# Kernel optimization log

Hardware: AMD Instinct MI355X
Metric: run time of the kernel (lower is better)

## Reference

```python
import jax, jax.numpy as jnp
import numpy as np
from jax.scipy.special import erf, erfc

B, D, C = 256, 512, 85742

def setup_inputs() -> dict:
    key = jax.random.key(0)
    k1, k2, k3, k4, k5 = jax.random.split(key, 5)
    x = jax.random.normal(k1, (B, D), dtype=jnp.float32)
    mu = jax.random.normal(k2, (B, D), dtype=jnp.float32)
    std = jax.random.uniform(k3, (B, D), dtype=jnp.float32)
    weight = jax.random.normal(k4, (C, D), dtype=jnp.float32)
    label = jax.random.randint(k5, (B,), 0, C, dtype=jnp.int64)
    return {"x": x, "mu": mu, "std": std, "weight": weight, "label": label}


def reference(x, mu, std, weight, label):
    # one_hot: [B, C] float, as in F.one_hot(...).float()
    one_hot = jax.nn.one_hot(label, weight.shape[0], dtype=jnp.float32)
    # wy = one_hot @ weight (embedding gather expressed as GEMM), wi = (1 - one_hot) @ weight
    wy = one_hot @ weight                 # [B, D]
    wi = (1.0 - one_hot) @ weight         # [B, D]
    sqrt2 = jnp.sqrt(jnp.float32(2.0))
    # torch.dist(a, b) is the scalar Frobenius (L2) distance
    dist_y = jnp.abs(jnp.sqrt(jnp.sum((wy - mu) ** 2)))
    dist_i = jnp.abs(jnp.sqrt(jnp.sum((wi - mu) ** 2)))
    erf_value = erf(dist_y / (sqrt2 * std))    # [B, D] via broadcast of scalar dist
    erfc_value = erfc(dist_i / (sqrt2 * std))  # [B, D]
    loss = erf_value.sum() + erfc_value.sum()
    return loss
```

## Files before the change

kernel.cpp:

```cpp
#include <hip/hip_runtime.h>
#include <math.h>

#define DDIM 512
#define BDIM 256
#define NCLS 85742
#define NB1 2048
#define CHUNK1 ((NCLS + NB1 - 1) / NB1)

typedef float f32x4 __attribute__((ext_vector_type(4)));

#define WS_UPART 1024
#define WS_PART  (1024 + 256 * 128 * 4)

__device__ __forceinline__ float wave_reduce(float v) {
    #pragma unroll
    for (int off = 32; off > 0; off >>= 1)
        v += __shfl_down(v, off, 64);
    return v;
}

__device__ __forceinline__ float block_reduce(float v, float* smem) {
    const int lane = threadIdx.x & 63;
    const int wid  = threadIdx.x >> 6;
    v = wave_reduce(v);
    if (lane == 0) smem[wid] = v;
    __syncthreads();
    if (wid == 0) {
        v = (lane < (int)(blockDim.x >> 6)) ? smem[lane] : 0.0f;
        v = wave_reduce(v);
    }
    return v;
}

__global__ __launch_bounds__(256, 4)
void colsum_partial(const float* __restrict__ W, const float* __restrict__ mu,
                    const int* __restrict__ label, float* __restrict__ ws,
                    float* __restrict__ out) {
    const int t = threadIdx.x;
    const int b = blockIdx.x;
    if (b == 0 && t == 0) { ws[0] = 0.0f; *out = 0.0f; }
    const int w = t >> 6, l = t & 63;
    const f32x4* __restrict__ W4 = reinterpret_cast<const f32x4*>(W);

    const int r0 = b * CHUNK1;
    const int r1 = (r0 + CHUNK1 < NCLS) ? (r0 + CHUNK1) : NCLS;
    const int rows = r1 - r0;

    __shared__ f32x4 smem[4][128];

    if (rows == CHUNK1) {
        const f32x4* base = W4 + ((size_t)r0 * 2 + w * 21) * 64 + l;
        f32x4 aE0 = (f32x4)(0.f), aE1 = aE0, aO0 = aE0, aO1 = aE0;
        f32x4 c0 = base[0], c1 = base[64], c2 = base[128], c3 = base[192];
        #pragma unroll
        for (int k = 1; k <= 4; ++k) {
            const f32x4* p = base + (size_t)k * 256;
            aE0 += c0;  c0 = p[0];
            aO0 += c1;  c1 = p[64];
            aE1 += c2;  c2 = p[128];
            aO1 += c3;  c3 = p[192];
        }
        f32x4 cl = base[1280];
        aE0 += c0; aO0 += c1; aE1 += c2; aO1 += c3;
        aE0 += cl;
        const int qE = (w & 1) * 64 + l;
        smem[w][qE]      = aE0 + aE1;
        smem[w][qE ^ 64] = aO0 + aO1;
    } else {
        const int q = t & 127, rsub = t >> 7;
        f32x4 a0 = (f32x4)(0.f);
        for (int r = r0 + rsub; r < r1; r += 2)
            a0 += W4[(size_t)r * 128 + q];
        smem[w][q]      = a0;
        smem[w][q ^ 64] = (f32x4)(0.f);
    }
    __syncthreads();
    if (t < 128) {
        f32x4 s = (smem[0][t] + smem[1][t]) + (smem[2][t] + smem[3][t]);
        f32x4* partialT = reinterpret_cast<f32x4*>(ws + WS_PART);
        partialT[(size_t)t * NB1 + b] = s;
    }

    if (b < 128) {
        const int q = t & 127, rsub = t >> 7;
        const int row = 2 * b + rsub;
        const int lab = label[row];
        const f32x4 m4 = reinterpret_cast<const f32x4*>(mu)[(size_t)row * 128 + q];
        const f32x4 w4 = W4[(size_t)lab * 128 + q];
        f32x4 d = w4 - m4;
        f32x4 u = w4 + m4;
        reinterpret_cast<f32x4*>(ws + WS_UPART)[(size_t)row * 128 + q] = u;
        float syp = d.x * d.x + d.y * d.y + d.z * d.z + d.w * d.w;
        float s2p = u.x * u.x + u.y * u.y + u.z * u.z + u.w * u.w;
        __shared__ float rsm[8];
        __syncthreads();
        syp = block_reduce(syp, rsm);
        __syncthreads();
        s2p = block_reduce(s2p, rsm);
        if (t == 0) {
            ws[16 + b]  = syp;
            ws[144 + b] = s2p;
        }
    }
}

__global__ __launch_bounds__(256, 4)
void reduce_kernel(float* __restrict__ ws) {
    const int q = blockIdx.x;
    const int t = threadIdx.x;
    const f32x4* __restrict__ partialT =
        reinterpret_cast<const f32x4*>(ws + WS_PART) + (size_t)q * NB1;
    f32x4 s = (f32x4)(0.f);
    #pragma unroll
    for (int k = 0; k < NB1 / 256; ++k)
        s += partialT[t + k * 256];
    f32x4 u = reinterpret_cast<const f32x4*>(ws + WS_UPART)[(size_t)t * 128 + q];

    float sx = wave_reduce(s.x), sy = wave_reduce(s.y);
    float sz = wave_reduce(s.z), sw = wave_reduce(s.w);
    float ux = wave_reduce(u.x), uy = wave_reduce(u.y);
    float uz = wave_reduce(u.z), uw = wave_reduce(u.w);
    __shared__ f32x4 sm[4], um[4];
    if ((t & 63) == 0) {
        sm[t >> 6] = (f32x4)(sx, sy, sz, sw);
        um[t >> 6] = (f32x4)(ux, uy, uz, uw);
    }
    __syncthreads();
    if (t == 0) {
        f32x4 cs = (sm[0] + sm[1]) + (sm[2] + sm[3]);
        f32x4 U  = (um[0] + um[1]) + (um[2] + um[3]);
        f32x4 si4 = 256.0f * cs * cs - 2.0f * cs * U;
        atomicAdd(&ws[0], si4.x + si4.y + si4.z + si4.w);
    }

    if (q == 0) {
        __syncthreads();
        __shared__ float rsm[8];
        float syp = (t < 128) ? ws[16 + t]  : 0.0f;
        float s2p = (t < 128) ? ws[144 + t] : 0.0f;
        syp = block_reduce(syp, rsm);
        __syncthreads();
        s2p = block_reduce(s2p, rsm);
        if (t == 0) { ws[1] = syp; ws[2] = s2p; }
    }
}

__global__ __launch_bounds__(256, 4)
void loss_kernel(const float* __restrict__ stdv, const float* __restrict__ ws,
                 float* __restrict__ out) {
    __shared__ float smem[8];
    const float dy = sqrtf(ws[1]);
    const float di = sqrtf(ws[0] + ws[2]);
    const float inv_sqrt2 = 0.70710678118654752f;
    const int i = blockIdx.x * 256 + threadIdx.x;
    f32x4 s4 = reinterpret_cast<const f32x4*>(stdv)[i];
    float acc;
    {
        float rx = inv_sqrt2 / s4.x, ry = inv_sqrt2 / s4.y;
        float rz = inv_sqrt2 / s4.z, rw = inv_sqrt2 / s4.w;
        acc  = erff(dy * rx) + erfcf(di * rx);
        acc += erff(dy * ry) + erfcf(di * ry);
        acc += erff(dy * rz) + erfcf(di * rz);
        acc += erff(dy * rw) + erfcf(di * rw);
    }
    acc = block_reduce(acc, smem);
    if (threadIdx.x == 0) atomicAdd(out, acc);
}

extern "C" void kernel_launch(void* const* d_in, const int* in_sizes, int n_in,
                              void* d_out, int out_size, void* d_ws, size_t ws_size,
                              hipStream_t stream) {
    const float* mu    = (const float*)d_in[1];
    const float* stdv  = (const float*)d_in[2];
    const float* W     = (const float*)d_in[3];
    const int*   label = (const int*)d_in[4];
    float* out = (float*)d_out;
    float* ws  = (float*)d_ws;

    colsum_partial<<<NB1, 256, 0, stream>>>(W, mu, label, ws, out);
    reduce_kernel<<<128, 256, 0, stream>>>(ws);
    loss_kernel<<<128, 256, 0, stream>>>(stdv, ws, out);
}
```

Measured before the change: 43.85 us.

## Stream weight column sums via 8-byte system-scope loads without LDS reduction

The column-sum kernel now has each thread own one float2 column pair and read rows with relaxed system-scope 64-bit atomic loads, likely so the loads bypass or change cache behaviour for the single-use stream. This drops the shared-memory cross-wave reduction and its barrier. Partials become float2 per thread, and the reduce kernel is relaunched with 256 blocks, each handling one float2 column pair. Narrower, system-scope loads may cost bandwidth or coalescing efficiency on the large weight stream.

```diff
diff --git a/kernel.cpp b/kernel.cpp
--- a/kernel.cpp
+++ b/kernel.cpp
@@ -8,6 +8,7 @@
 #define CHUNK1 ((NCLS + NB1 - 1) / NB1)
 
 typedef float f32x4 __attribute__((ext_vector_type(4)));
+typedef float f32x2 __attribute__((ext_vector_type(2)));
 
 #define WS_UPART 1024
 #define WS_PART  (1024 + 256 * 128 * 4)
@@ -32,6 +33,12 @@
     return v;
 }
 
+__device__ __forceinline__ f32x2 ldsys(const unsigned long long* p) {
+    unsigned long long v = __hip_atomic_load(p, __ATOMIC_RELAXED,
+                                             __HIP_MEMORY_SCOPE_SYSTEM);
+    return __builtin_bit_cast(f32x2, v);
+}
+
 __global__ __launch_bounds__(256, 4)
 void colsum_partial(const float* __restrict__ W, const float* __restrict__ mu,
                     const int* __restrict__ label, float* __restrict__ ws,
@@ -39,61 +46,54 @@
     const int t = threadIdx.x;
     const int b = blockIdx.x;
     if (b == 0 && t == 0) { ws[0] = 0.0f; *out = 0.0f; }
-    const int w = t >> 6, l = t & 63;
-    const f32x4* __restrict__ W4 = reinterpret_cast<const f32x4*>(W);
+
+    const unsigned long long* __restrict__ Wu =
+        reinterpret_cast<const unsigned long long*>(W);
 
     const int r0 = b * CHUNK1;
     const int r1 = (r0 + CHUNK1 < NCLS) ? (r0 + CHUNK1) : NCLS;
     const int rows = r1 - r0;
 
-    __shared__ f32x4 smem[4][128];
+    f32x2 a0 = (f32x2)(0.f), a1 = a0, a2 = a0, a3 = a0;
+    const unsigned long long* base = Wu + (size_t)r0 * 256 + t;
 
     if (rows == CHUNK1) {
-        const f32x4* base = W4 + ((size_t)r0 * 2 + w * 21) * 64 + l;
-        f32x4 aE0 = (f32x4)(0.f), aE1 = aE0, aO0 = aE0, aO1 = aE0;
-        f32x4 c0 = base[0], c1 = base[64], c2 = base[128], c3 = base[192];
+        f32x2 c0 = ldsys(base);
+        f32x2 c1 = ldsys(base + 256);
+        f32x2 c2 = ldsys(base + 512);
+        f32x2 c3 = ldsys(base + 768);
         #pragma unroll
-        for (int k = 1; k <= 4; ++k) {
-            const f32x4* p = base + (size_t)k * 256;
-            aE0 += c0;  c0 = p[0];
-            aO0 += c1;  c1 = p[64];
-            aE1 += c2;  c2 = p[128];
-            aO1 += c3;  c3 = p[192];
+        for (int k = 1; k <= 9; ++k) {
+            const unsigned long long* p = base + (size_t)k * 1024;
+            a0 += c0;  c0 = ldsys(p);
+            a1 += c1;  c1 = ldsys(p + 256);
+            a2 += c2;  c2 = ldsys(p + 512);
+            a3 += c3;  c3 = ldsys(p + 768);
         }
-        f32x4 cl = base[1280];
-        aE0 += c0; aO0 += c1; aE1 += c2; aO1 += c3;
-        aE0 += cl;
-        const int qE = (w & 1) * 64 + l;
-        smem[w][qE]      = aE0 + aE1;
-        smem[w][qE ^ 64] = aO0 + aO1;
+        a0 += c0; a1 += c1; a2 += c2; a3 += c3;
+        a0 += ldsys(base + 10240);
+        a1 += ldsys(base + 10496);
     } else {
-        const int q = t & 127, rsub = t >> 7;
-        f32x4 a0 = (f32x4)(0.f);
-        for (int r = r0 + rsub; r < r1; r += 2)
-            a0 += W4[(size_t)r * 128 + q];
-        smem[w][q]      = a0;
-        smem[w][q ^ 64] = (f32x4)(0.f);
+        for (int r = 0; r < rows; ++r)
+            a0 += ldsys(base + (size_t)r * 256);
     }
-    __syncthreads();
-    if (t < 128) {
-        f32x4 s = (smem[0][t] + smem[1][t]) + (smem[2][t] + smem[3][t]);
-        f32x4* partialT = reinterpret_cast<f32x4*>(ws + WS_PART);
-        partialT[(size_t)t * NB1 + b] = s;
-    }
+    a0 += a1 + a2 + a3;
+
+    f32x2* partial2 = reinterpret_cast<f32x2*>(ws + WS_PART);
+    partial2[(size_t)t * NB1 + b] = a0;
 
     if (b < 128) {
         const int q = t & 127, rsub = t >> 7;
         const int row = 2 * b + rsub;
         const int lab = label[row];
         const f32x4 m4 = reinterpret_cast<const f32x4*>(mu)[(size_t)row * 128 + q];
-        const f32x4 w4 = W4[(size_t)lab * 128 + q];
+        const f32x4 w4 = reinterpret_cast<const f32x4*>(W)[(size_t)lab * 128 + q];
         f32x4 d = w4 - m4;
         f32x4 u = w4 + m4;
         reinterpret_cast<f32x4*>(ws + WS_UPART)[(size_t)row * 128 + q] = u;
         float syp = d.x * d.x + d.y * d.y + d.z * d.z + d.w * d.w;
         float s2p = u.x * u.x + u.y * u.y + u.z * u.z + u.w * u.w;
         __shared__ float rsm[8];
-        __syncthreads();
         syp = block_reduce(syp, rsm);
         __syncthreads();
         s2p = block_reduce(s2p, rsm);
@@ -106,36 +106,29 @@
 
 __global__ __launch_bounds__(256, 4)
 void reduce_kernel(float* __restrict__ ws) {
-    const int q = blockIdx.x;
+    const int cp = blockIdx.x;
     const int t = threadIdx.x;
-    const f32x4* __restrict__ partialT =
-        reinterpret_cast<const f32x4*>(ws + WS_PART) + (size_t)q * NB1;
-    f32x4 s = (f32x4)(0.f);
+    const f32x2* __restrict__ partial2 =
+        reinterpret_cast<const f32x2*>(ws + WS_PART) + (size_t)cp * NB1;
+    f32x2 s = (f32x2)(0.f);
     #pragma unroll
     for (int k = 0; k < NB1 / 256; ++k)
-        s += partialT[t + k * 256];
-    f32x4 u = reinterpret_cast<const f32x4*>(ws + WS_UPART)[(size_t)t * 128 + q];
+        s += partial2[t + k * 256];
+    const f32x4 u4 = reinterpret_cast<const f32x4*>(ws + WS_UPART)[(size_t)t * 128 + (cp >> 1)];
+    const f32x2 u2 = (cp & 1) ? u4.zw : u4.xy;
 
-    float sx = wave_reduce(s.x), sy = wave_reduce(s.y);
-    float sz = wave_reduce(s.z), sw = wave_reduce(s.w);
-    float ux = wave_reduce(u.x), uy = wave_reduce(u.y);
-    float uz = wave_reduce(u.z), uw = wave_reduce(u.w);
-    __shared__ f32x4 sm[4], um[4];
-    if ((t & 63) == 0) {
-        sm[t >> 6] = (f32x4)(sx, sy, sz, sw);
-        um[t >> 6] = (f32x4)(ux, uy, uz, uw);
-    }
-    __syncthreads();
+    __shared__ float rsm[8];
+    float csx = block_reduce(s.x, rsm);  __syncthreads();
+    float csy = block_reduce(s.y, rsm);  __syncthreads();
+    float Ux  = block_reduce(u2.x, rsm); __syncthreads();
+    float Uy  = block_reduce(u2.y, rsm);
     if (t == 0) {
-        f32x4 cs = (sm[0] + sm[1]) + (sm[2] + sm[3]);
-        f32x4 U  = (um[0] + um[1]) + (um[2] + um[3]);
-        f32x4 si4 = 256.0f * cs * cs - 2.0f * cs * U;
-        atomicAdd(&ws[0], si4.x + si4.y + si4.z + si4.w);
+        float si = 256.0f * (csx * csx + csy * csy) - 2.0f * (csx * Ux + csy * Uy);
+        atomicAdd(&ws[0], si);
     }
 
-    if (q == 0) {
+    if (cp == 0) {
         __syncthreads();
-        __shared__ float rsm[8];
         float syp = (t < 128) ? ws[16 + t]  : 0.0f;
         float s2p = (t < 128) ? ws[144 + t] : 0.0f;
         syp = block_reduce(syp, rsm);
@@ -178,6 +171,6 @@
     float* ws  = (float*)d_ws;
 
     colsum_partial<<<NB1, 256, 0, stream>>>(W, mu, label, ws, out);
-    reduce_kernel<<<128, 256, 0, stream>>>(ws);
+    reduce_kernel<<<256, 256, 0, stream>>>(ws);
     loss_kernel<<<128, 256, 0, stream>>>(stdv, ws, out);
 }
```

Result: slower. 49.00 us (+11.7%).
